# Kernel optimization log

Measured on AMD Instinct MI355X. Metric: run time of the kernel, lower is better.

## Reference

```python
import jax, jax.numpy as jnp
import numpy as np

B, C, H, W = 16, 512, 32, 32
NH = 8
HD = C // NH  # 64


def setup_inputs() -> dict:
    key = jax.random.key(0)
    ks = jax.random.split(key, 9)
    s = 1.0 / np.sqrt(C)
    return {
        "x": jax.random.normal(ks[0], (B, C, H, W), dtype=jnp.float32),
        "Wq": jax.random.normal(ks[1], (C, C), dtype=jnp.float32) * s,
        "bq": jnp.zeros((C,), dtype=jnp.float32),
        "Wk": jax.random.normal(ks[2], (C, C), dtype=jnp.float32) * s,
        "bk": jnp.zeros((C,), dtype=jnp.float32),
        "Wv": jax.random.normal(ks[3], (C, C), dtype=jnp.float32) * s,
        "bv": jnp.zeros((C,), dtype=jnp.float32),
        "Wo": jax.random.normal(ks[4], (C, C), dtype=jnp.float32) * s,
        "bo": jnp.zeros((C,), dtype=jnp.float32),
    }


def reference(x, Wq, bq, Wk, bk, Wv, bv, Wo, bo):
    b, c, h, w = x.shape
    n = h * w  # sequence of spatial tokens
    # [B, C, H, W] -> [B, N, C]
    xf = x.reshape(b, c, n).transpose(0, 2, 1)
    # separate QKV projections, split heads: [B, NH, N, HD]
    def split_heads(t):
        return t.reshape(b, n, NH, HD).transpose(0, 2, 1, 3)
    q = split_heads(xf @ Wq + bq)
    k = split_heads(xf @ Wk + bk)
    v = split_heads(xf @ Wv + bv)
    # energy: [B, NH, N, N]
    energy = jnp.einsum('bhqd,bhkd->bhqk', q, k) / jnp.sqrt(jnp.float32(HD))
    attn = jax.nn.softmax(energy, axis=-1)
    out = jnp.einsum('bhqk,bhkd->bhqd', attn, v)  # [B, NH, N, HD]
    out = out.transpose(0, 2, 1, 3).reshape(b, n, c)
    out = out @ Wo + bo
    return out.transpose(0, 2, 1).reshape(b, c, h, w)
```

## Files before the change

kernel.cpp:

```cpp
#include <hip/hip_runtime.h>
#include <hip/hip_bf16.h>
#include <math.h>

constexpr int B_  = 16;
constexpr int C_  = 512;
constexpr int N_  = 1024;
constexpr int NH_ = 8;
constexpr int HD_ = 64;

#define QSCALE 0.18033688f

typedef __attribute__((ext_vector_type(8))) short short8;
typedef __attribute__((ext_vector_type(4))) short short4v;
typedef __attribute__((ext_vector_type(4))) float f32x4;
#define MFMA16(a, b, c) __builtin_amdgcn_mfma_f32_16x16x32_bf16((a), (b), (c), 0, 0, 0)

#if __has_builtin(__builtin_amdgcn_exp2f)
#define EXP2(x) __builtin_amdgcn_exp2f(x)
#else
#define EXP2(x) exp2f(x)
#endif

__device__ __forceinline__ short f2bf(float f) {
    union { float f; unsigned u; } a; a.f = f;
    unsigned r = a.u + 0x7fffu + ((a.u >> 16) & 1u);
    return (short)(r >> 16);
}
__device__ __forceinline__ short f2bf_hw(float f) {
    __hip_bfloat16 h = __float2bfloat16(f);
    return *reinterpret_cast<short*>(&h);
}

__device__ __forceinline__ void gload_lds16(const void* g, void* l) {
    __builtin_amdgcn_global_load_lds(
        (const __attribute__((address_space(1))) unsigned*)g,
        (__attribute__((address_space(3))) unsigned*)l, 16, 0, 0);
}

__global__ __launch_bounds__(256) void prep_x(const float* __restrict__ x,
                                              short* __restrict__ xt) {
    const int wgid = blockIdx.x;
    const int xcd = wgid & 7;
    const int i = wgid >> 3;
    const int b  = 2 * xcd + (i >= 128);
    const int tile = i & 127;
    const int tn = tile >> 3;
    const int tc = tile & 7;
    __shared__ float t[64][65];
    const int tid = threadIdx.x;
    #pragma unroll
    for (int k = 0; k < 16; ++k) {
        int idx = k * 256 + tid;
        int r = idx >> 6, col = idx & 63;
        t[r][col] = x[((size_t)b * C_ + tc * 64 + r) * N_ + tn * 64 + col];
    }
    __syncthreads();
    #pragma unroll
    for (int k = 0; k < 16; ++k) {
        int idx = k * 256 + tid;
        int r2 = idx >> 6, col2 = idx & 63;
        xt[((size_t)b * N_ + tn * 64 + r2) * C_ + tc * 64 + col2] = f2bf(t[col2][r2]);
    }
}

__global__ __launch_bounds__(256) void prep_w(
    const float* __restrict__ Wq, const float* __restrict__ Wk,
    const float* __restrict__ Wv, const float* __restrict__ Wo,
    short* __restrict__ WqT, short* __restrict__ WkT,
    short* __restrict__ WvT, short* __restrict__ WoT) {
    const int z = blockIdx.y;
    const float* W = (z == 0) ? Wq : (z == 1) ? Wk : (z == 2) ? Wv : Wo;
    short* WT      = (z == 0) ? WqT : (z == 1) ? WkT : (z == 2) ? WvT : WoT;
    const int tco = blockIdx.x / (C_ / 64);
    const int tc  = blockIdx.x % (C_ / 64);
    __shared__ float t[64][65];
    const int tid = threadIdx.x;
    #pragma unroll
    for (int i = 0; i < 16; ++i) {
        int idx = i * 256 + tid;
        int r = idx >> 6, col = idx & 63;
        t[r][col] = W[((size_t)tc * 64 + r) * C_ + tco * 64 + col];
    }
    __syncthreads();
    #pragma unroll
    for (int i = 0; i < 16; ++i) {
        int idx = i * 256 + tid;
        int r2 = idx >> 6, col2 = idx & 63;
        WT[((size_t)tco * 64 + r2) * C_ + tc * 64 + col2] = f2bf(t[col2][r2]);
    }
}

#define GEMM_STAGE(buf, t)                                                    \
    {                                                                         \
        _Pragma("unroll")                                                     \
        for (int ii = 0; ii < 4; ++ii) {                                      \
            gload_lds16(Ag + arowoff + (size_t)ii * 8 * C_ + (t) * 64,        \
                        &smem[buf][0][wave * 32 + ii * 8][0]);                \
            gload_lds16(Bg + arowoff + (size_t)ii * 8 * C_ + (t) * 64,        \
                        &smem[buf][1][wave * 32 + ii * 8][0]);                \
        }                                                                     \
    }

#define GEMM_CORE()                                                           \
    GEMM_STAGE(0, 0);                                                         \
    __syncthreads();                                                          \
    for (int t = 0; t < 8; ++t) {                                             \
        const int buf = t & 1;                                                \
        if (t < 7) GEMM_STAGE(buf ^ 1, t + 1);                                \
        __builtin_amdgcn_s_setprio(1);                                        \
        _Pragma("unroll")                                                     \
        for (int ks = 0; ks < 2; ++ks) {                                      \
            short8 af[4], bf[4];                                              \
            const int sw = ((ks * 4 + g) ^ (c & 7)) << 3;                     \
            _Pragma("unroll")                                                 \
            for (int fm = 0; fm < 4; ++fm)                                    \
                af[fm] = *(const short8*)&smem[buf][0][wm * 64 + fm * 16 + c][sw]; \
            _Pragma("unroll")                                                 \
            for (int fn = 0; fn < 4; ++fn)                                    \
                bf[fn] = *(const short8*)&smem[buf][1][wn * 64 + fn * 16 + c][sw]; \
            _Pragma("unroll")                                                 \
            for (int fm = 0; fm < 4; ++fm)                                    \
                _Pragma("unroll")                                             \
                for (int fn = 0; fn < 4; ++fn)                                \
                    acc[fm][fn] = MFMA16(af[fm], bf[fn], acc[fm][fn]);        \
        }                                                                     \
        __builtin_amdgcn_s_setprio(0);                                        \
        __syncthreads();                                                      \
    }

__global__ __launch_bounds__(256) void qkv_mfma(
    const short* __restrict__ xt,
    const short* __restrict__ WqT, const float* __restrict__ bq,
    const short* __restrict__ WkT, const float* __restrict__ bk,
    const short* __restrict__ WvT, const float* __restrict__ bv,
    short* __restrict__ Qs, short* __restrict__ Kb, short* __restrict__ Vt) {
    const int wgid = blockIdx.x;
    const int xcd = wgid & 7;
    const int i = wgid >> 3;
    const int b = 2 * xcd + (i >= 96);
    const int rem = (i >= 96) ? i - 96 : i;
    const int z = rem >> 5;
    const int tile = rem & 31;
    const int mt = tile >> 2;
    const int nt = tile & 3;
    const int tid = threadIdx.x;
    const int wave = tid >> 6, lane = tid & 63;
    const int g = lane >> 4, c = lane & 15;
    const int wm = wave >> 1, wn = wave & 1;

    const short* W    = (z == 0) ? WqT : (z == 1) ? WkT : WvT;
    const float* bias = (z == 0) ? bq  : (z == 1) ? bk  : bv;

    __shared__ __align__(16) short smem[2][2][128][64];

    const short* Ag = xt + (size_t)b * N_ * C_ + (size_t)mt * 128 * C_;
    const short* Bg = W + (size_t)nt * 128 * C_;

    const int lrow = lane >> 3, lslot = lane & 7;
    const size_t arowoff = (size_t)(wave * 32 + lrow) * C_ + ((lslot ^ lrow) << 3);

    f32x4 acc[4][4] = {};
    GEMM_CORE();

    const int tok0 = mt * 128 + wm * 64;
    const int co0  = nt * 128 + wn * 64;
    const int h = co0 >> 6;
    const size_t bh = (size_t)(b * NH_ + h);

    if (z < 2) {
        short* Y = (z == 0) ? Qs : Kb;
        const float sc = (z == 0) ? QSCALE : 1.f;
        #pragma unroll
        for (int fm = 0; fm < 4; ++fm)
            #pragma unroll
            for (int fn = 0; fn < 4; ++fn)
                #pragma unroll
                for (int r = 0; r < 4; ++r) {
                    int tok = tok0 + fm * 16 + 4 * g + r;
                    int hd  = fn * 16 + c;
                    float v = (acc[fm][fn][r] + bias[co0 + hd]) * sc;
                    Y[(bh * N_ + tok) * HD_ + hd] = f2bf_hw(v);
                }
    } else {
        short (*t72)[72] = (short(*)[72])((short*)smem + wave * 32 * 72);
        #pragma unroll
        for (int p = 0; p < 2; ++p) {
            #pragma unroll
            for (int fn2 = 0; fn2 < 2; ++fn2) {
                int fnn = 2 * p + fn2;
                #pragma unroll
                for (int fm = 0; fm < 4; ++fm) {
                    short4v pk;
                    #pragma unroll
                    for (int r = 0; r < 4; ++r)
                        pk[r] = f2bf_hw(acc[fm][fnn][r] + bias[co0 + fnn * 16 + c]);
                    *(short4v*)&t72[fn2 * 16 + c][fm * 16 + 4 * g] = pk;
                }
            }
            int row = lane >> 1, half2 = lane & 1;
            int hd = p * 32 + row;
            size_t base = (bh * HD_ + hd) * N_ + tok0 + half2 * 32;
            #pragma unroll
            for (int j = 0; j < 4; ++j)
                *(short8*)&Vt[base + j * 8] = *(const short8*)&t72[row][half2 * 32 + j * 8];
        }
    }
}

__global__ __launch_bounds__(512) void attn_mfma(
    const short* __restrict__ Qs, const short* __restrict__ Kb,
    const short* __restrict__ Vt, short* __restrict__ Ah) {
    const int wgid = blockIdx.x;
    const int swz  = (wgid & 7) * 64 + (wgid >> 3);
    const int b  = swz >> 5;
    const int h  = (swz >> 2) & 7;
    const int qt = swz & 3;
    const int tid = threadIdx.x;
    const int wave = tid >> 6, lane = tid & 63;
    const int g = lane >> 4, c = lane & 15;
    const int q0 = qt * 256 + wave * 32;
    const size_t bh = (size_t)(b * NH_ + h);

    const short* Qw  = Qs + (bh * N_ + q0) * HD_;
    const short* Kbb = Kb + bh * N_ * HD_;
    const short* Vtb = Vt + bh * HD_ * N_;

    __shared__ short KV[2][2][4096];
    __shared__ short Pl[8][32][64];
    short (*P)[64] = Pl[wave];
    const int px = (c & 7) << 1;

    const int srow = tid >> 3;
    const int sc16 = tid & 7;
    const int kdst = srow * 64 + 8 * (sc16 ^ (srow & 7));
    short8 gk, gv;

    #define STAGE_LOAD(key0)                                                   \
        do {                                                                   \
            gk = *(const short8*)&Kbb[(size_t)((key0) + srow) * HD_ + sc16 * 8]; \
            gv = *(const short8*)&Vtb[(size_t)srow * N_ + (key0) + sc16 * 8];    \
        } while (0)
    #define STAGE_WRITE(buf)                                                   \
        do {                                                                   \
            *(short8*)&KV[buf][0][kdst] = gk;                                  \
            *(short8*)&KV[buf][1][kdst] = gv;                                  \
        } while (0)

    short8 qf[2][2];
    #pragma unroll
    for (int f = 0; f < 2; ++f)
        #pragma unroll
        for (int k0 = 0; k0 < 2; ++k0)
            qf[f][k0] = *(const short8*)&Qw[(f * 16 + c) * HD_ + k0 * 32 + g * 8];

    short8 ones8;
    #pragma unroll
    for (int j = 0; j < 8; ++j) ones8[j] = (short)0x3F80;

    f32x4 o[2][4] = {};
    f32x4 lacc[2] = {};

    STAGE_LOAD(0);
    STAGE_WRITE(0);
    STAGE_LOAD(64);
    __syncthreads();

    int cur = 0;
    for (int it = 0; it < 16; ++it) {
        if (it < 15) STAGE_WRITE(cur ^ 1);
        if (it < 14) STAGE_LOAD((it + 2) * 64);

        const short* Kl = &KV[cur][0][0];
        const short* Vl = &KV[cur][1][0];

        f32x4 s[2][4] = {};
        __builtin_amdgcn_s_setprio(1);
        #pragma unroll
        for (int m = 0; m < 4; ++m) {
            const int row = m * 16 + c;
            short8 ka = *(const short8*)&Kl[row * 64 + 8 * ((g)     ^ (row & 7))];
            short8 kb = *(const short8*)&Kl[row * 64 + 8 * ((4 + g) ^ (row & 7))];
            s[0][m] = MFMA16(ka, qf[0][0], s[0][m]);
            s[0][m] = MFMA16(kb, qf[0][1], s[0][m]);
            s[1][m] = MFMA16(ka, qf[1][0], s[1][m]);
            s[1][m] = MFMA16(kb, qf[1][1], s[1][m]);
        }
        __builtin_amdgcn_s_setprio(0);

        #pragma unroll
        for (int f = 0; f < 2; ++f) {
            #pragma unroll
            for (int m = 0; m < 4; ++m) {
                short4v pk;
                #pragma unroll
                for (int r = 0; r < 4; ++r) pk[r] = f2bf_hw(EXP2(s[f][m][r]));
                *(short4v*)&P[f * 16 + c][((4 * m + g) ^ px) * 4] = pk;
            }
        }

        short8 pa[2][2];
        #pragma unroll
        for (int f = 0; f < 2; ++f)
            #pragma unroll
            for (int k0 = 0; k0 < 2; ++k0)
                pa[f][k0] = *(const short8*)&P[f * 16 + c][((k0 * 8 + 2 * g) ^ px) * 4];
        __builtin_amdgcn_s_setprio(1);
        lacc[0] = MFMA16(pa[0][0], ones8, lacc[0]);
        lacc[0] = MFMA16(pa[0][1], ones8, lacc[0]);
        lacc[1] = MFMA16(pa[1][0], ones8, lacc[1]);
        lacc[1] = MFMA16(pa[1][1], ones8, lacc[1]);
        #pragma unroll
        for (int n = 0; n < 4; ++n) {
            const int row = n * 16 + c;
            short8 va = *(const short8*)&Vl[row * 64 + 8 * ((g)     ^ (row & 7))];
            short8 vb = *(const short8*)&Vl[row * 64 + 8 * ((4 + g) ^ (row & 7))];
            o[0][n] = MFMA16(pa[0][0], va, o[0][n]);
            o[0][n] = MFMA16(pa[0][1], vb, o[0][n]);
            o[1][n] = MFMA16(pa[1][0], va, o[1][n]);
            o[1][n] = MFMA16(pa[1][1], vb, o[1][n]);
        }
        __builtin_amdgcn_s_setprio(0);

        __syncthreads();
        cur ^= 1;
    }
    #undef STAGE_LOAD
    #undef STAGE_WRITE

    #pragma unroll
    for (int f = 0; f < 2; ++f) {
        float li[4];
        #pragma unroll
        for (int r = 0; r < 4; ++r) li[r] = 1.f / lacc[f][r];
        #pragma unroll
        for (int n = 0; n < 4; ++n)
            #pragma unroll
            for (int r = 0; r < 4; ++r) {
                int tok = q0 + f * 16 + 4 * g + r;
                int cc  = h * 64 + n * 16 + c;
                Ah[((size_t)b * N_ + tok) * C_ + cc] = f2bf_hw(o[f][n][r] * li[r]);
            }
    }
}

__global__ __launch_bounds__(256) void proj_mfma(
    const short* __restrict__ Ah, const short* __restrict__ WoT,
    const float* __restrict__ bo, float* __restrict__ out) {
    const int wgid = blockIdx.x;
    const int xcd = wgid & 7;
    const int i = wgid >> 3;
    const int b = 2 * xcd + (i >= 32);
    const int tile = i & 31;
    const int mt = tile >> 2;
    const int nt = tile & 3;
    const int tid = threadIdx.x;
    const int wave = tid >> 6, lane = tid & 63;
    const int g = lane >> 4, c = lane & 15;
    const int wm = wave >> 1, wn = wave & 1;

    __shared__ __align__(16) short smem[2][2][128][64];

    const short* Ag = Ah + (size_t)b * N_ * C_ + (size_t)mt * 128 * C_;
    const short* Bg = WoT + (size_t)nt * 128 * C_;

    const int lrow = lane >> 3, lslot = lane & 7;
    const size_t arowoff = (size_t)(wave * 32 + lrow) * C_ + ((lslot ^ lrow) << 3);

    f32x4 acc[4][4] = {};
    GEMM_CORE();

    const int tok0 = mt * 128 + wm * 64;
    const int co0  = nt * 128 + wn * 64;

    float (*tf)[68] = (float(*)[68])((float*)smem + wave * 32 * 68);
    #pragma unroll
    for (int p = 0; p < 2; ++p) {
        #pragma unroll
        for (int fm = 0; fm < 4; ++fm)
            #pragma unroll
            for (int fn2 = 0; fn2 < 2; ++fn2) {
                float4 v = *(float4*)&acc[fm][2 * p + fn2];
                *(float4*)&tf[fn2 * 16 + c][fm * 16 + 4 * g] = v;
            }
        int row = lane >> 1, half = lane & 1;
        int co = co0 + p * 32 + row;
        float bias = bo[co];
        float* ob = out + ((size_t)b * C_ + co) * N_ + tok0 + half * 32;
        #pragma unroll
        for (int j = 0; j < 8; ++j) {
            float4 v = *(const float4*)&tf[row][half * 32 + j * 4];
            v.x += bias; v.y += bias; v.z += bias; v.w += bias;
            *(float4*)&ob[j * 4] = v;
        }
    }
}

extern "C" void kernel_launch(void* const* d_in, const int* in_sizes, int n_in,
                              void* d_out, int out_size, void* d_ws, size_t ws_size,
                              hipStream_t stream) {
    (void)in_sizes; (void)n_in; (void)out_size; (void)ws_size;
    const float* x  = (const float*)d_in[0];
    const float* Wq = (const float*)d_in[1];
    const float* bq = (const float*)d_in[2];
    const float* Wk = (const float*)d_in[3];
    const float* bk = (const float*)d_in[4];
    const float* Wv = (const float*)d_in[5];
    const float* bv = (const float*)d_in[6];
    const float* Wo = (const float*)d_in[7];
    const float* bo = (const float*)d_in[8];
    float* out = (float*)d_out;

    char* ws = (char*)d_ws;
    const size_t MB = 1024 * 1024;
    short* xt  = (short*)(ws + 0 * MB);
    short* WqT = (short*)(ws + 16 * MB);
    short* WkT = (short*)(ws + 16 * MB + 512 * 1024);
    short* WvT = (short*)(ws + 17 * MB);
    short* WoT = (short*)(ws + 17 * MB + 512 * 1024);
    short* Qsb = (short*)(ws + 18 * MB);
    short* Kb  = (short*)(ws + 34 * MB);
    short* Vt  = (short*)(ws + 50 * MB);
    short* Ah  = (short*)(ws + 66 * MB);

    prep_x<<<dim3(2048), 256, 0, stream>>>(x, xt);
    prep_w<<<dim3(64, 4), 256, 0, stream>>>(Wq, Wk, Wv, Wo, WqT, WkT, WvT, WoT);
    qkv_mfma<<<dim3(1536), 256, 0, stream>>>(xt, WqT, bq, WkT, bk, WvT, bv,
                                             Qsb, Kb, Vt);
    attn_mfma<<<dim3(512), 512, 0, stream>>>(Qsb, Kb, Vt, Ah);
    proj_mfma<<<dim3(512), 256, 0, stream>>>(Ah, WoT, bo, out);
}
```

Measured before the change: 110.8 us.

## Merge prep kernels and shrink attention blocks to four waves with register staging

New measurement: 118.7 us. 1.07x slower.

```diff
diff --git a/kernel.cpp b/kernel.cpp
--- a/kernel.cpp
+++ b/kernel.cpp
@@ -37,56 +37,56 @@
         (__attribute__((address_space(3))) unsigned*)l, 16, 0, 0);
 }
 
-__global__ __launch_bounds__(256) void prep_x(const float* __restrict__ x,
-                                              short* __restrict__ xt) {
-    const int wgid = blockIdx.x;
-    const int xcd = wgid & 7;
-    const int i = wgid >> 3;
-    const int b  = 2 * xcd + (i >= 128);
-    const int tile = i & 127;
-    const int tn = tile >> 3;
-    const int tc = tile & 7;
-    __shared__ float t[64][65];
-    const int tid = threadIdx.x;
-    #pragma unroll
-    for (int k = 0; k < 16; ++k) {
-        int idx = k * 256 + tid;
-        int r = idx >> 6, col = idx & 63;
-        t[r][col] = x[((size_t)b * C_ + tc * 64 + r) * N_ + tn * 64 + col];
-    }
-    __syncthreads();
-    #pragma unroll
-    for (int k = 0; k < 16; ++k) {
-        int idx = k * 256 + tid;
-        int r2 = idx >> 6, col2 = idx & 63;
-        xt[((size_t)b * N_ + tn * 64 + r2) * C_ + tc * 64 + col2] = f2bf(t[col2][r2]);
-    }
-}
-
-__global__ __launch_bounds__(256) void prep_w(
+__global__ __launch_bounds__(256) void prep_all(
+    const float* __restrict__ x, short* __restrict__ xt,
     const float* __restrict__ Wq, const float* __restrict__ Wk,
     const float* __restrict__ Wv, const float* __restrict__ Wo,
     short* __restrict__ WqT, short* __restrict__ WkT,
     short* __restrict__ WvT, short* __restrict__ WoT) {
-    const int z = blockIdx.y;
-    const float* W = (z == 0) ? Wq : (z == 1) ? Wk : (z == 2) ? Wv : Wo;
-    short* WT      = (z == 0) ? WqT : (z == 1) ? WkT : (z == 2) ? WvT : WoT;
-    const int tco = blockIdx.x / (C_ / 64);
-    const int tc  = blockIdx.x % (C_ / 64);
     __shared__ float t[64][65];
     const int tid = threadIdx.x;
-    #pragma unroll
-    for (int i = 0; i < 16; ++i) {
-        int idx = i * 256 + tid;
-        int r = idx >> 6, col = idx & 63;
-        t[r][col] = W[((size_t)tc * 64 + r) * C_ + tco * 64 + col];
-    }
-    __syncthreads();
-    #pragma unroll
-    for (int i = 0; i < 16; ++i) {
-        int idx = i * 256 + tid;
-        int r2 = idx >> 6, col2 = idx & 63;
-        WT[((size_t)tco * 64 + r2) * C_ + tc * 64 + col2] = f2bf(t[col2][r2]);
+    const int wgid = blockIdx.x;
+    if (wgid < 2048) {
+        const int xcd = wgid & 7;
+        const int i = wgid >> 3;
+        const int b  = 2 * xcd + (i >= 128);
+        const int tile = i & 127;
+        const int tn = tile >> 3;
+        const int tc = tile & 7;
+        #pragma unroll
+        for (int k = 0; k < 16; ++k) {
+            int idx = k * 256 + tid;
+            int r = idx >> 6, col = idx & 63;
+            t[r][col] = x[((size_t)b * C_ + tc * 64 + r) * N_ + tn * 64 + col];
+        }
+        __syncthreads();
+        #pragma unroll
+        for (int k = 0; k < 16; ++k) {
+            int idx = k * 256 + tid;
+            int r2 = idx >> 6, col2 = idx & 63;
+            xt[((size_t)b * N_ + tn * 64 + r2) * C_ + tc * 64 + col2] = f2bf(t[col2][r2]);
+        }
+    } else {
+        const int idx0 = wgid - 2048;
+        const int z = idx0 >> 6;
+        const float* W = (z == 0) ? Wq : (z == 1) ? Wk : (z == 2) ? Wv : Wo;
+        short* WT      = (z == 0) ? WqT : (z == 1) ? WkT : (z == 2) ? WvT : WoT;
+        const int tile = idx0 & 63;
+        const int tco = tile >> 3;
+        const int tc  = tile & 7;
+        #pragma unroll
+        for (int i = 0; i < 16; ++i) {
+            int idx = i * 256 + tid;
+            int r = idx >> 6, col = idx & 63;
+            t[r][col] = W[((size_t)tc * 64 + r) * C_ + tco * 64 + col];
+        }
+        __syncthreads();
+        #pragma unroll
+        for (int i = 0; i < 16; ++i) {
+            int idx = i * 256 + tid;
+            int r2 = idx >> 6, col2 = idx & 63;
+            WT[((size_t)tco * 64 + r2) * C_ + tc * 64 + col2] = f2bf(t[col2][r2]);
+        }
     }
 }
 
@@ -207,43 +207,50 @@
     }
 }
 
-__global__ __launch_bounds__(512) void attn_mfma(
+__global__ __launch_bounds__(256) void attn_mfma(
     const short* __restrict__ Qs, const short* __restrict__ Kb,
     const short* __restrict__ Vt, short* __restrict__ Ah) {
     const int wgid = blockIdx.x;
-    const int swz  = (wgid & 7) * 64 + (wgid >> 3);
-    const int b  = swz >> 5;
-    const int h  = (swz >> 2) & 7;
-    const int qt = swz & 3;
+    const int swz  = (wgid & 7) * 128 + (wgid >> 3);
+    const int b  = swz >> 6;
+    const int h  = (swz >> 3) & 7;
+    const int qt = swz & 7;
     const int tid = threadIdx.x;
     const int wave = tid >> 6, lane = tid & 63;
     const int g = lane >> 4, c = lane & 15;
-    const int q0 = qt * 256 + wave * 32;
+    const int q0 = qt * 128 + wave * 32;
     const size_t bh = (size_t)(b * NH_ + h);
 
     const short* Qw  = Qs + (bh * N_ + q0) * HD_;
     const short* Kbb = Kb + bh * N_ * HD_;
     const short* Vtb = Vt + bh * HD_ * N_;
 
-    __shared__ short KV[2][2][4096];
-    __shared__ short Pl[8][32][64];
+    __shared__ short KV[2][4096];
+    __shared__ short Pl[4][32][64];
     short (*P)[64] = Pl[wave];
     const int px = (c & 7) << 1;
 
     const int srow = tid >> 3;
     const int sc16 = tid & 7;
-    const int kdst = srow * 64 + 8 * (sc16 ^ (srow & 7));
-    short8 gk, gv;
-
-    #define STAGE_LOAD(key0)                                                   \
+    const int sswz = 8 * (sc16 ^ (srow & 7));
+    const int kdst0 = srow * 64 + sswz;
+    const int kdst1 = (srow + 32) * 64 + sswz;
+
+    short8 Ak0, Ak1, Av0, Av1, Bk0, Bk1, Bv0, Bv1;
+
+    #define STAGE_LOAD(S, key0)                                                \
         do {                                                                   \
-            gk = *(const short8*)&Kbb[(size_t)((key0) + srow) * HD_ + sc16 * 8]; \
-            gv = *(const short8*)&Vtb[(size_t)srow * N_ + (key0) + sc16 * 8];    \
+            S##k0 = *(const short8*)&Kbb[(size_t)((key0) + srow) * HD_ + sc16 * 8];      \
+            S##k1 = *(const short8*)&Kbb[(size_t)((key0) + srow + 32) * HD_ + sc16 * 8]; \
+            S##v0 = *(const short8*)&Vtb[(size_t)srow * N_ + (key0) + sc16 * 8];         \
+            S##v1 = *(const short8*)&Vtb[(size_t)(srow + 32) * N_ + (key0) + sc16 * 8];  \
         } while (0)
-    #define STAGE_WRITE(buf)                                                   \
+    #define STAGE_WRITE(S)                                                     \
         do {                                                                   \
-            *(short8*)&KV[buf][0][kdst] = gk;                                  \
-            *(short8*)&KV[buf][1][kdst] = gv;                                  \
+            *(short8*)&KV[0][kdst0] = S##k0;                                   \
+            *(short8*)&KV[0][kdst1] = S##k1;                                   \
+            *(short8*)&KV[1][kdst0] = S##v0;                                   \
+            *(short8*)&KV[1][kdst1] = S##v1;                                   \
         } while (0)
 
     short8 qf[2][2];
@@ -260,72 +267,79 @@
     f32x4 o[2][4] = {};
     f32x4 lacc[2] = {};
 
-    STAGE_LOAD(0);
-    STAGE_WRITE(0);
-    STAGE_LOAD(64);
+    #define COMPUTE_CHUNK()                                                    \
+    {                                                                          \
+        const short* Kl = &KV[0][0];                                           \
+        const short* Vl = &KV[1][0];                                           \
+        f32x4 s[2][4] = {};                                                    \
+        __builtin_amdgcn_s_setprio(1);                                         \
+        _Pragma("unroll")                                                      \
+        for (int m = 0; m < 4; ++m) {                                          \
+            const int row = m * 16 + c;                                        \
+            short8 ka = *(const short8*)&Kl[row * 64 + 8 * ((g)     ^ (row & 7))]; \
+            short8 kb = *(const short8*)&Kl[row * 64 + 8 * ((4 + g) ^ (row & 7))]; \
+            s[0][m] = MFMA16(ka, qf[0][0], s[0][m]);                           \
+            s[0][m] = MFMA16(kb, qf[0][1], s[0][m]);                           \
+            s[1][m] = MFMA16(ka, qf[1][0], s[1][m]);                           \
+            s[1][m] = MFMA16(kb, qf[1][1], s[1][m]);                           \
+        }                                                                      \
+        __builtin_amdgcn_s_setprio(0);                                         \
+        _Pragma("unroll")                                                      \
+        for (int f = 0; f < 2; ++f) {                                          \
+            _Pragma("unroll")                                                  \
+            for (int m = 0; m < 4; ++m) {                                      \
+                short4v pk;                                                    \
+                _Pragma("unroll")                                              \
+                for (int r = 0; r < 4; ++r) pk[r] = f2bf_hw(EXP2(s[f][m][r])); \
+                *(short4v*)&P[f * 16 + c][((4 * m + g) ^ px) * 4] = pk;        \
+            }                                                                  \
+        }                                                                      \
+        short8 pa[2][2];                                                       \
+        _Pragma("unroll")                                                      \
+        for (int f = 0; f < 2; ++f)                                            \
+            _Pragma("unroll")                                                  \
+            for (int k0 = 0; k0 < 2; ++k0)                                     \
+                pa[f][k0] = *(const short8*)&P[f * 16 + c][((k0 * 8 + 2 * g) ^ px) * 4]; \
+        __builtin_amdgcn_s_setprio(1);                                         \
+        lacc[0] = MFMA16(pa[0][0], ones8, lacc[0]);                            \
+        lacc[0] = MFMA16(pa[0][1], ones8, lacc[0]);                            \
+        lacc[1] = MFMA16(pa[1][0], ones8, lacc[1]);                            \
+        lacc[1] = MFMA16(pa[1][1], ones8, lacc[1]);                            \
+        _Pragma("unroll")                                                      \
+        for (int n = 0; n < 4; ++n) {                                          \
+            const int row = n * 16 + c;                                        \
+            short8 va = *(const short8*)&Vl[row * 64 + 8 * ((g)     ^ (row & 7))]; \
+            short8 vb = *(const short8*)&Vl[row * 64 + 8 * ((4 + g) ^ (row & 7))]; \
+            o[0][n] = MFMA16(pa[0][0], va, o[0][n]);                           \
+            o[0][n] = MFMA16(pa[0][1], vb, o[0][n]);                           \
+            o[1][n] = MFMA16(pa[1][0], va, o[1][n]);                           \
+            o[1][n] = MFMA16(pa[1][1], vb, o[1][n]);                           \
+        }                                                                      \
+        __builtin_amdgcn_s_setprio(0);                                         \
+    }
+
+    STAGE_LOAD(A, 0);
+    STAGE_WRITE(A);
+    STAGE_LOAD(B, 64);
     __syncthreads();
 
-    int cur = 0;
-    for (int it = 0; it < 16; ++it) {
-        if (it < 15) STAGE_WRITE(cur ^ 1);
-        if (it < 14) STAGE_LOAD((it + 2) * 64);
-
-        const short* Kl = &KV[cur][0][0];
-        const short* Vl = &KV[cur][1][0];
-
-        f32x4 s[2][4] = {};
-        __builtin_amdgcn_s_setprio(1);
-        #pragma unroll
-        for (int m = 0; m < 4; ++m) {
-            const int row = m * 16 + c;
-            short8 ka = *(const short8*)&Kl[row * 64 + 8 * ((g)     ^ (row & 7))];
-            short8 kb = *(const short8*)&Kl[row * 64 + 8 * ((4 + g) ^ (row & 7))];
-            s[0][m] = MFMA16(ka, qf[0][0], s[0][m]);
-            s[0][m] = MFMA16(kb, qf[0][1], s[0][m]);
-            s[1][m] = MFMA16(ka, qf[1][0], s[1][m]);
-            s[1][m] = MFMA16(kb, qf[1][1], s[1][m]);
-        }
-        __builtin_amdgcn_s_setprio(0);
-
-        #pragma unroll
-        for (int f = 0; f < 2; ++f) {
-            #pragma unroll
-            for (int m = 0; m < 4; ++m) {
-                short4v pk;
-                #pragma unroll
-                for (int r = 0; r < 4; ++r) pk[r] = f2bf_hw(EXP2(s[f][m][r]));
-                *(short4v*)&P[f * 16 + c][((4 * m + g) ^ px) * 4] = pk;
-            }
-        }
-
-        short8 pa[2][2];
-        #pragma unroll
-        for (int f = 0; f < 2; ++f)
-            #pragma unroll
-            for (int k0 = 0; k0 < 2; ++k0)
-                pa[f][k0] = *(const short8*)&P[f * 16 + c][((k0 * 8 + 2 * g) ^ px) * 4];
-        __builtin_amdgcn_s_setprio(1);
-        lacc[0] = MFMA16(pa[0][0], ones8, lacc[0]);
-        lacc[0] = MFMA16(pa[0][1], ones8, lacc[0]);
-        lacc[1] = MFMA16(pa[1][0], ones8, lacc[1]);
-        lacc[1] = MFMA16(pa[1][1], ones8, lacc[1]);
-        #pragma unroll
-        for (int n = 0; n < 4; ++n) {
-            const int row = n * 16 + c;
-            short8 va = *(const short8*)&Vl[row * 64 + 8 * ((g)     ^ (row & 7))];
-            short8 vb = *(const short8*)&Vl[row * 64 + 8 * ((4 + g) ^ (row & 7))];
-            o[0][n] = MFMA16(pa[0][0], va, o[0][n]);
-            o[0][n] = MFMA16(pa[0][1], vb, o[0][n]);
-            o[1][n] = MFMA16(pa[1][0], va, o[1][n]);
-            o[1][n] = MFMA16(pa[1][1], vb, o[1][n]);
-        }
-        __builtin_amdgcn_s_setprio(0);
-
-        __syncthreads();
-        cur ^= 1;
+    for (int i2 = 0; i2 < 8; ++i2) {
+        if (i2 < 7) STAGE_LOAD(A, (2 * i2 + 2) * 64);
+        COMPUTE_CHUNK();
+        __syncthreads();
+        STAGE_WRITE(B);
+        __syncthreads();
+        if (i2 < 7) STAGE_LOAD(B, (2 * i2 + 3) * 64);
+        COMPUTE_CHUNK();
+        __syncthreads();
+        if (i2 < 7) {
+            STAGE_WRITE(A);
+        }
+        __syncthreads();
     }
     #undef STAGE_LOAD
     #undef STAGE_WRITE
+    #undef COMPUTE_CHUNK
 
     #pragma unroll
     for (int f = 0; f < 2; ++f) {
@@ -422,10 +436,10 @@
     short* Vt  = (short*)(ws + 50 * MB);
     short* Ah  = (short*)(ws + 66 * MB);
 
-    prep_x<<<dim3(2048), 256, 0, stream>>>(x, xt);
-    prep_w<<<dim3(64, 4), 256, 0, stream>>>(Wq, Wk, Wv, Wo, WqT, WkT, WvT, WoT);
+    prep_all<<<dim3(2304), 256, 0, stream>>>(x, xt, Wq, Wk, Wv, Wo,
+                                             WqT, WkT, WvT, WoT);
     qkv_mfma<<<dim3(1536), 256, 0, stream>>>(xt, WqT, bq, WkT, bk, WvT, bv,
                                              Qsb, Kb, Vt);
-    attn_mfma<<<dim3(512), 512, 0, stream>>>(Qsb, Kb, Vt, Ah);
+    attn_mfma<<<dim3(1024), 256, 0, stream>>>(Qsb, Kb, Vt, Ah);
     proj_mfma<<<dim3(512), 256, 0, stream>>>(Ah, WoT, bo, out);
 }
```
